# Kernel tuning notes

Measured on AMD Instinct MI355X. Metric: run time of the kernel, lower is better.

Reference implementation:

```python
import jax, jax.numpy as jnp
import numpy as np

D_MODEL = 1024
D_FF = 4096
LN_EPS = 1e-5


def setup_inputs() -> dict:
    key = jax.random.key(0)
    k_x, k_w1, k_w2 = jax.random.split(key, 3)
    x = jax.random.normal(k_x, (4, 2048, D_MODEL), dtype=jnp.float32)
    # LayerNorm affine params (torch defaults: weight=1, bias=0)
    ln_w = jnp.ones((D_MODEL,), dtype=jnp.float32)
    ln_b = jnp.zeros((D_MODEL,), dtype=jnp.float32)
    # Linear layers, torch default init: U(-1/sqrt(fan_in), 1/sqrt(fan_in))
    lim1 = 1.0 / np.sqrt(D_MODEL)
    w1 = jax.random.uniform(k_w1, (D_MODEL, D_FF), minval=-lim1, maxval=lim1, dtype=jnp.float32)
    b1 = jnp.zeros((D_FF,), dtype=jnp.float32)
    lim2 = 1.0 / np.sqrt(D_FF)
    w2 = jax.random.uniform(k_w2, (D_FF, D_MODEL), minval=-lim2, maxval=lim2, dtype=jnp.float32)
    b2 = jnp.zeros((D_MODEL,), dtype=jnp.float32)
    return {"x": x, "ln_w": ln_w, "ln_b": ln_b, "w1": w1, "b1": b1, "w2": w2, "b2": b2}


def reference(x, ln_w, ln_b, w1, b1, w2, b2):
    # LayerNorm over last dim
    mu = jnp.mean(x, axis=-1, keepdims=True)
    var = jnp.mean(jnp.square(x - mu), axis=-1, keepdims=True)
    h = (x - mu) * jax.lax.rsqrt(var + LN_EPS) * ln_w + ln_b
    # Linear -> ReLU -> Linear
    h = jnp.maximum(jnp.einsum('bsd,df->bsf', h, w1) + b1, 0.0)
    return jnp.einsum('bsf,fd->bsd', h, w2) + b2
```

## Files before the change

kernel.cpp:

```cpp
#include <hip/hip_runtime.h>
#include <stdint.h>

#define D_MODEL 1024
#define D_FF    4096
#define NROWS   8192

typedef __attribute__((ext_vector_type(4))) float f32x4;
typedef __attribute__((ext_vector_type(8))) short short8;

__device__ __forceinline__ unsigned short f2bf(float f) {
  unsigned u = __float_as_uint(f);
  u += 0x7fffu + ((u >> 16) & 1u);
  return (unsigned short)(u >> 16);
}

template <int N>
__device__ __forceinline__ void wait_vmcnt() {
  asm volatile("s_waitcnt vmcnt(%0)" ::"n"(N) : "memory");
}

__global__ __launch_bounds__(256) void ln_bf16_kernel(
    const float* __restrict__ x, const float* __restrict__ lnw,
    const float* __restrict__ lnb, unsigned short* __restrict__ y) {
  const int row = blockIdx.x;
  const int t = threadIdx.x;
  const int w = t >> 6, l = t & 63;
  const float4* xr = (const float4*)(x + (size_t)row * D_MODEL);
  float4 v = xr[t];
  float s  = v.x + v.y + v.z + v.w;
  float s2 = v.x * v.x + v.y * v.y + v.z * v.z + v.w * v.w;
#pragma unroll
  for (int o = 32; o >= 1; o >>= 1) {
    s  += __shfl_xor(s, o);
    s2 += __shfl_xor(s2, o);
  }
  __shared__ float red[8];
  if (l == 0) { red[w] = s; red[4 + w] = s2; }
  __syncthreads();
  s  = red[0] + red[1] + red[2] + red[3];
  s2 = red[4] + red[5] + red[6] + red[7];
  const float mu  = s * (1.0f / D_MODEL);
  const float var = s2 * (1.0f / D_MODEL) - mu * mu;
  const float rs  = rsqrtf(var + 1e-5f);
  float4 wv = ((const float4*)lnw)[t];
  float4 bv = ((const float4*)lnb)[t];
  ushort4 o4;
  o4.x = f2bf((v.x - mu) * rs * wv.x + bv.x);
  o4.y = f2bf((v.y - mu) * rs * wv.y + bv.y);
  o4.z = f2bf((v.z - mu) * rs * wv.z + bv.z);
  o4.w = f2bf((v.w - mu) * rs * wv.w + bv.w);
  *(ushort4*)(y + (size_t)row * D_MODEL + t * 4) = o4;
}

__global__ __launch_bounds__(256) void transpose_f32_bf16(
    const float* __restrict__ src, unsigned short* __restrict__ dst,
    int R, int C) {
  __shared__ float tile[32][33];
  const int tx = threadIdx.x;
  const int ty = threadIdx.y;
  const int r0 = blockIdx.y * 32, c0 = blockIdx.x * 32;
#pragma unroll
  for (int i = 0; i < 32; i += 8)
    tile[ty + i][tx] = src[(size_t)(r0 + ty + i) * C + (c0 + tx)];
  __syncthreads();
#pragma unroll
  for (int i = 0; i < 32; i += 8)
    dst[(size_t)(c0 + ty + i) * R + (r0 + tx)] = f2bf(tile[tx][ty + i]);
}

template <int BN, int RELU, int BF16OUT>
__global__ __launch_bounds__(512, 2) void gemm8p(
    const unsigned short* __restrict__ A, const unsigned short* __restrict__ Bt,
    const float* __restrict__ bias, unsigned short* __restrict__ Cb,
    float* __restrict__ Cf, int M, int N, int K) {
  constexpr int BM = 256;
  constexpr int FN = BN / 64;
  constexpr int FNH = FN / 2;
  constexpr int LA = 2;
  constexpr int LB = BN / 128;
  constexpr int AH = 128 * 64;
  constexpr int BH = (BN / 2) * 64;
  constexpr int BUFSZ = 2 * AH + 2 * BH;
  constexpr int RPW = BN / 8;
  constexpr int WTN = BN / 4;
  constexpr int NW_A = 2 * LA + LB;
  constexpr int NW_B = LA + 2 * LB;

  __shared__ short lds[2 * BUFSZ];

  const int t = threadIdx.x;
  const int w = t >> 6, l = t & 63;
  const int wm = w >> 2, wn = w & 3;
  const int lr = l & 15, lg = l >> 4, l7 = l & 7;
  const int wm64 = wm * 64, wnr = wn * RPW;

  const int gx = gridDim.x;
  const int nwg = gx * gridDim.y;
  int id = blockIdx.y * gx + blockIdx.x;
  id = (id & 7) * (nwg >> 3) + (id >> 3);
  const int bn0 = (id % gx) * BN;
  const int bm0 = (id / gx) * BM;

  f32x4 acc[8][FN];
#pragma unroll
  for (int i = 0; i < 8; ++i)
#pragma unroll
    for (int j = 0; j < FN; ++j) acc[i][j] = (f32x4){0.f, 0.f, 0.f, 0.f};

  auto stageA = [&](int buf, int mq, int kt) {
#pragma unroll
    for (int i = 0; i < LA; ++i) {
      const int idx = i * 512 + t;
      const int r = idx >> 3;
      const int sl = (idx & 7) ^ (r & 7);
      const int grow = bm0 + ((r >> 6) << 7) + (mq << 6) + (r & 63);
      __builtin_amdgcn_global_load_lds(
          (const __attribute__((address_space(1))) void*)(A + (size_t)grow * K + kt * 64 + sl * 8),
          (__attribute__((address_space(3))) void*)(&lds[buf * BUFSZ + mq * AH + idx * 8]),
          16, 0, 0);
    }
  };
  auto stageB = [&](int buf, int nq, int kt) {
#pragma unroll
    for (int i = 0; i < LB; ++i) {
      const int idx = i * 512 + t;
      const int r = idx >> 3;
      const int sl = (idx & 7) ^ (r & 7);
      const int grow = bn0 + (r / RPW) * WTN + nq * RPW + (r % RPW);
      __builtin_amdgcn_global_load_lds(
          (const __attribute__((address_space(1))) void*)(Bt + (size_t)grow * K + kt * 64 + sl * 8),
          (__attribute__((address_space(3))) void*)(&lds[buf * BUFSZ + 2 * AH + nq * BH + idx * 8]),
          16, 0, 0);
    }
  };

#define PHASE(MQ, NQ, BUFR, NWAIT, STAGESTMT)                                  \
  {                                                                            \
    wait_vmcnt<NWAIT>();                                                       \
    short8 af[2][4];                                                           \
    short8 bv[2][FNH];                                                         \
    _Pragma("unroll") for (int ks = 0; ks < 2; ++ks) {                         \
      const int sw = (ks << 2) | lg;                                           \
      _Pragma("unroll") for (int f = 0; f < 4; ++f)                            \
        af[ks][f] = *(const short8*)&lds[(BUFR) * BUFSZ + (MQ) * AH +          \
                                         (wm64 + f * 16 + lr) * 64 +           \
                                         ((sw ^ l7) << 3)];                    \
      _Pragma("unroll") for (int f = 0; f < FNH; ++f)                          \
        bv[ks][f] = *(const short8*)&lds[(BUFR) * BUFSZ + 2 * AH + (NQ) * BH + \
                                         (wnr + f * 16 + lr) * 64 +            \
                                         ((sw ^ l7) << 3)];                    \
    }                                                                          \
    STAGESTMT;                                                                 \
    __builtin_amdgcn_s_barrier();                                              \
    asm volatile("s_waitcnt lgkmcnt(0)" ::: "memory");                         \
    __builtin_amdgcn_sched_barrier(0);                                         \
    __builtin_amdgcn_s_setprio(1);                                             \
    _Pragma("unroll") for (int ks = 0; ks < 2; ++ks)                           \
      _Pragma("unroll") for (int f = 0; f < 4; ++f)                            \
        _Pragma("unroll") for (int g = 0; g < FNH; ++g)                        \
          acc[(MQ) * 4 + f][(NQ) * FNH + g] =                                  \
              __builtin_amdgcn_mfma_f32_16x16x32_bf16(                         \
                  af[ks][f], bv[ks][g], acc[(MQ) * 4 + f][(NQ) * FNH + g],     \
                  0, 0, 0);                                                    \
    __builtin_amdgcn_s_setprio(0);                                             \
    __builtin_amdgcn_sched_barrier(0);                                         \
    __builtin_amdgcn_s_barrier();                                              \
  }

  const int KT_MAX = (K >> 6) - 1;
  const int NIT = K >> 7;

  stageA(0, 0, 0);
  stageB(0, 0, 0);
  stageB(0, 1, 0);
  stageA(0, 1, 0);
  stageA(1, 0, 1);
  stageB(1, 0, 1);
  wait_vmcnt<2 * LA + 2 * LB>();
  __builtin_amdgcn_s_barrier();

  for (int it = 0; it < NIT; ++it) {
    const int k1 = 2 * it + 1;
    int k2 = 2 * it + 2; k2 = k2 > KT_MAX ? KT_MAX : k2;
    int k3 = 2 * it + 3; k3 = k3 > KT_MAX ? KT_MAX : k3;
    PHASE(0, 0, 0, NW_A, stageB(1, 1, k1));
    PHASE(0, 1, 0, NW_B, stageA(1, 1, k1));
    PHASE(1, 0, 0, NW_B, stageA(0, 0, k2));
    PHASE(1, 1, 0, NW_A, stageB(0, 0, k2));
    PHASE(0, 0, 1, NW_A, stageB(0, 1, k2));
    PHASE(0, 1, 1, NW_B, stageA(0, 1, k2));
    PHASE(1, 0, 1, NW_B, stageA(1, 0, k3));
    PHASE(1, 1, 1, NW_A, stageB(1, 0, k3));
  }
#undef PHASE
  asm volatile("s_waitcnt vmcnt(0)" ::: "memory");

#pragma unroll
  for (int fn = 0; fn < FN; ++fn) {
    const int col = bn0 + wn * WTN + fn * 16 + lr;
    const float bvs = bias[col];
#pragma unroll
    for (int fm = 0; fm < 8; ++fm) {
      const int rb = bm0 + wm * 128 + fm * 16 + lg * 4;
#pragma unroll
      for (int j = 0; j < 4; ++j) {
        float v = acc[fm][fn][j] + bvs;
        if (RELU) v = v > 0.f ? v : 0.f;
        if (BF16OUT) Cb[(size_t)(rb + j) * N + col] = f2bf(v);
        else         Cf[(size_t)(rb + j) * N + col] = v;
      }
    }
  }
}

extern "C" void kernel_launch(void* const* d_in, const int* in_sizes, int n_in,
                              void* d_out, int out_size, void* d_ws, size_t ws_size,
                              hipStream_t stream) {
  const float* x   = (const float*)d_in[0];
  const float* lnw = (const float*)d_in[1];
  const float* lnb = (const float*)d_in[2];
  const float* w1  = (const float*)d_in[3];
  const float* b1  = (const float*)d_in[4];
  const float* w2  = (const float*)d_in[5];
  const float* b2  = (const float*)d_in[6];
  float* out = (float*)d_out;

  char* ws = (char*)d_ws;
  unsigned short* x_ln = (unsigned short*)(ws);
  unsigned short* w1t  = (unsigned short*)(ws + (16u << 20));
  unsigned short* w2t  = (unsigned short*)(ws + (24u << 20));
  unsigned short* h    = (unsigned short*)(ws + (32u << 20));

  ln_bf16_kernel<<<NROWS, 256, 0, stream>>>(x, lnw, lnb, x_ln);
  transpose_f32_bf16<<<dim3(D_FF / 32, D_MODEL / 32), dim3(32, 8), 0, stream>>>(
      w1, w1t, D_MODEL, D_FF);
  transpose_f32_bf16<<<dim3(D_MODEL / 32, D_FF / 32), dim3(32, 8), 0, stream>>>(
      w2, w2t, D_FF, D_MODEL);
  gemm8p<256, 1, 1><<<dim3(D_FF / 256, NROWS / 256), 512, 0, stream>>>(
      x_ln, w1t, b1, h, nullptr, NROWS, D_FF, D_MODEL);
  gemm8p<128, 0, 0><<<dim3(D_MODEL / 128, NROWS / 256), 512, 0, stream>>>(
      h, w2t, b2, nullptr, out, NROWS, D_MODEL, D_FF);
}
```

Baseline: 277.5 us.

## Reuse LDS fragments across GEMM phases via snake phase ordering

Reorders the four per-buffer GEMM phases in a snake pattern (00,01,11,10) so that A fragments are reused across consecutive phases and B fragments for both N halves stay in registers. This cuts the LDS reads per buffer roughly in half. The cost is more live registers (two sets of B fragments), which under launch_bounds(512,2) could cause spills or tighter scheduling. It also relies on the LDS buffer not being overwritten while its fragments are still held in registers.

```diff
diff --git a/kernel.cpp b/kernel.cpp
--- a/kernel.cpp
+++ b/kernel.cpp
@@ -69,7 +69,7 @@
 }
 
 template <int BN, int RELU, int BF16OUT>
-__global__ __launch_bounds__(512, 2) void gemm8p(
+__global__ __launch_bounds__(512, 2) void gemm8s(
     const unsigned short* __restrict__ A, const unsigned short* __restrict__ Bt,
     const float* __restrict__ bias, unsigned short* __restrict__ Cb,
     float* __restrict__ Cf, int M, int N, int K) {
@@ -107,6 +107,9 @@
 #pragma unroll
     for (int j = 0; j < FN; ++j) acc[i][j] = (f32x4){0.f, 0.f, 0.f, 0.f};
 
+  short8 af[2][4];
+  short8 bq[2][2][FNH];
+
   auto stageA = [&](int buf, int mq, int kt) {
 #pragma unroll
     for (int i = 0; i < LA; ++i) {
@@ -134,21 +137,21 @@
     }
   };
 
-#define PHASE(MQ, NQ, BUFR, NWAIT, STAGESTMT)                                  \
+#define PHASE(MQ, NQ, BUFR, NWAIT, LDA_, LDB_, STAGESTMT)                      \
   {                                                                            \
     wait_vmcnt<NWAIT>();                                                       \
-    short8 af[2][4];                                                           \
-    short8 bv[2][FNH];                                                         \
-    _Pragma("unroll") for (int ks = 0; ks < 2; ++ks) {                         \
-      const int sw = (ks << 2) | lg;                                           \
-      _Pragma("unroll") for (int f = 0; f < 4; ++f)                            \
-        af[ks][f] = *(const short8*)&lds[(BUFR) * BUFSZ + (MQ) * AH +          \
-                                         (wm64 + f * 16 + lr) * 64 +           \
-                                         ((sw ^ l7) << 3)];                    \
-      _Pragma("unroll") for (int f = 0; f < FNH; ++f)                          \
-        bv[ks][f] = *(const short8*)&lds[(BUFR) * BUFSZ + 2 * AH + (NQ) * BH + \
-                                         (wnr + f * 16 + lr) * 64 +            \
-                                         ((sw ^ l7) << 3)];                    \
+    if (LDA_) {                                                                \
+      _Pragma("unroll") for (int ks = 0; ks < 2; ++ks)                         \
+        _Pragma("unroll") for (int f = 0; f < 4; ++f)                          \
+          af[ks][f] = *(const short8*)&lds[(BUFR) * BUFSZ + (MQ) * AH +        \
+              (wm64 + f * 16 + lr) * 64 + ((((ks << 2) | lg) ^ l7) << 3)];     \
+    }                                                                          \
+    if (LDB_) {                                                                \
+      _Pragma("unroll") for (int ks = 0; ks < 2; ++ks)                         \
+        _Pragma("unroll") for (int g = 0; g < FNH; ++g)                        \
+          bq[NQ][ks][g] = *(const short8*)&lds[(BUFR) * BUFSZ + 2 * AH +       \
+              (NQ) * BH + (wnr + g * 16 + lr) * 64 +                           \
+              ((((ks << 2) | lg) ^ l7) << 3)];                                 \
     }                                                                          \
     STAGESTMT;                                                                 \
     __builtin_amdgcn_s_barrier();                                              \
@@ -160,7 +163,7 @@
         _Pragma("unroll") for (int g = 0; g < FNH; ++g)                        \
           acc[(MQ) * 4 + f][(NQ) * FNH + g] =                                  \
               __builtin_amdgcn_mfma_f32_16x16x32_bf16(                         \
-                  af[ks][f], bv[ks][g], acc[(MQ) * 4 + f][(NQ) * FNH + g],     \
+                  af[ks][f], bq[NQ][ks][g], acc[(MQ) * 4 + f][(NQ) * FNH + g], \
                   0, 0, 0);                                                    \
     __builtin_amdgcn_s_setprio(0);                                             \
     __builtin_amdgcn_sched_barrier(0);                                         \
@@ -183,14 +186,14 @@
     const int k1 = 2 * it + 1;
     int k2 = 2 * it + 2; k2 = k2 > KT_MAX ? KT_MAX : k2;
     int k3 = 2 * it + 3; k3 = k3 > KT_MAX ? KT_MAX : k3;
-    PHASE(0, 0, 0, NW_A, stageB(1, 1, k1));
-    PHASE(0, 1, 0, NW_B, stageA(1, 1, k1));
-    PHASE(1, 0, 0, NW_B, stageA(0, 0, k2));
-    PHASE(1, 1, 0, NW_A, stageB(0, 0, k2));
-    PHASE(0, 0, 1, NW_A, stageB(0, 1, k2));
-    PHASE(0, 1, 1, NW_B, stageA(0, 1, k2));
-    PHASE(1, 0, 1, NW_B, stageA(1, 0, k3));
-    PHASE(1, 1, 1, NW_A, stageB(1, 0, k3));
+    PHASE(0, 0, 0, NW_A, 1, 1, stageB(1, 1, k1));
+    PHASE(0, 1, 0, NW_B, 0, 1, stageA(1, 1, k1));
+    PHASE(1, 1, 0, NW_B, 1, 0, stageA(0, 0, k2));
+    PHASE(1, 0, 0, NW_A, 0, 0, stageB(0, 0, k2));
+    PHASE(0, 0, 1, NW_A, 1, 1, stageB(0, 1, k2));
+    PHASE(0, 1, 1, NW_B, 0, 1, stageA(0, 1, k2));
+    PHASE(1, 1, 1, NW_B, 1, 0, stageA(1, 0, k3));
+    PHASE(1, 0, 1, NW_A, 0, 0, stageB(1, 0, k3));
   }
 #undef PHASE
   asm volatile("s_waitcnt vmcnt(0)" ::: "memory");
@@ -236,8 +239,8 @@
       w1, w1t, D_MODEL, D_FF);
   transpose_f32_bf16<<<dim3(D_MODEL / 32, D_FF / 32), dim3(32, 8), 0, stream>>>(
       w2, w2t, D_FF, D_MODEL);
-  gemm8p<256, 1, 1><<<dim3(D_FF / 256, NROWS / 256), 512, 0, stream>>>(
+  gemm8s<256, 1, 1><<<dim3(D_FF / 256, NROWS / 256), 512, 0, stream>>>(
       x_ln, w1t, b1, h, nullptr, NROWS, D_FF, D_MODEL);
-  gemm8p<128, 0, 0><<<dim3(D_MODEL / 128, NROWS / 256), 512, 0, stream>>>(
+  gemm8s<128, 0, 0><<<dim3(D_MODEL / 128, NROWS / 256), 512, 0, stream>>>(
       h, w2t, b2, nullptr, out, NROWS, D_MODEL, D_FF);
 }
```

After: 261.1 us. 5.9% less time.
